# Kernel tuning notes

Hardware: AMD Instinct MI355X
Metric: run time of the kernel (lower is better)

Reference implementation:

```python
import jax, jax.numpy as jnp
import numpy as np
from jax import lax

EPS = 0.1
MAX_ITER = 100
THRESH = 0.01
N = 4  # number of prompt ensembles


def _l2norm(x, axis):
    return x / jnp.linalg.norm(x, axis=axis, keepdims=True)


def sinkhorn(K, u, v, max_iter=MAX_ITER, thresh=THRESH):
    # K: [B, M, N], u: [B, M], v: [B, N]. Matches torch loop with early exit
    # on mean(|r - r0|) < thresh, done on-device via lax.while_loop.
    dt = K.dtype
    r0 = jnp.ones_like(u)
    c0 = jnp.ones_like(v)

    def cond(state):
        _, _, i, err = state
        return jnp.logical_and(i < max_iter, err >= thresh)

    def body(state):
        r, c, i, _ = state
        r_new = u / jnp.einsum('bmn,bn->bm', K, c)
        c_new = v / jnp.einsum('bmn,bm->bn', K, r_new)
        err = jnp.mean(jnp.abs(r_new - r))
        return (r_new, c_new, i + 1, err)

    r, c, _, _ = lax.while_loop(cond, body, (r0, c0, jnp.int32(0), jnp.asarray(jnp.inf, dt)))
    # T = outer(r, c) * K
    return r[:, :, None] * c[:, None, :] * K


def setup_inputs() -> dict:
    key = jax.random.key(0)
    k1, k2, k3 = jax.random.split(key, 3)
    M, b, d = 196, 32, 512
    n_cls = 1000
    return {
        'image_features': jax.random.normal(k1, (M, b, d), dtype=jnp.float32),
        'image_feature_pool': jax.random.normal(k2, (b, d), dtype=jnp.float32),
        'text_features': jax.random.normal(k3, (N * n_cls, d), dtype=jnp.float32),
        'logit_scale': jnp.asarray(np.log(1.0 / 0.07), dtype=jnp.float32),
    }


def reference(image_features, image_feature_pool, text_features, logit_scale):
    M, b, d = image_features.shape
    n_cls = text_features.shape[0] // N

    tf = text_features.reshape(N, n_cls, d)
    text_feature_pool = tf.mean(axis=0)

    imf = _l2norm(image_features, axis=2)          # [M, b, d]
    img_pool = _l2norm(image_feature_pool, axis=1)  # [b, d]
    tfn = _l2norm(tf, axis=2)                       # [N, n_cls, d]
    txt_pool = _l2norm(text_feature_pool, axis=1)   # [n_cls, d]

    # sim: [M, N, b, n_cls] -> [M, N, b*n_cls] -> [B, M, N]
    sim = jnp.einsum('mbd,ncd->mnbc', imf, tfn)
    sim = sim.reshape(M, N, b * n_cls).transpose(2, 0, 1)
    wdist = 1.0 - sim

    B = b * n_cls
    xx = jnp.full((B, M), 1.0 / M, dtype=sim.dtype)
    yy = jnp.full((B, N), 1.0 / N, dtype=sim.dtype)

    # torch.no_grad() around Sinkhorn -> stop gradients into the iteration
    K = jnp.exp(-lax.stop_gradient(wdist) / EPS)
    T = sinkhorn(K, xx, yy)

    sim_op = jnp.sum(T * sim, axis=(1, 2)).reshape(b, n_cls)

    ls = jnp.exp(logit_scale)
    logits = ls * (img_pool @ txt_pool.T)
    logits2 = 0.5 * (ls * sim_op) + 0.5 * logits
    return logits2
```

## Files before the change

kernel.cpp:

```cpp
#include <hip/hip_runtime.h>
#include <hip/hip_bf16.h>

#define MB 6272
#define NC 4000
#define DD 512
#define NCLS 1000
#define NB 32000
#define NITER 6
#define SK_STRIDE 68

typedef __attribute__((ext_vector_type(8))) short short8;
typedef __attribute__((ext_vector_type(4))) float f32x4;
typedef __attribute__((ext_vector_type(2))) float f32x2;

__device__ __forceinline__ float bflo(unsigned u) { return __builtin_bit_cast(float, u << 16); }
__device__ __forceinline__ float bfhi(unsigned u) { return __builtin_bit_cast(float, u & 0xFFFF0000u); }
__device__ __forceinline__ float frcp(float x) { return __builtin_amdgcn_rcpf(x); }

__device__ __forceinline__ unsigned short f2bf(float x) {
  unsigned u = __builtin_bit_cast(unsigned, x);
  u += 0x7FFFu + ((u >> 16) & 1u);
  return (unsigned short)(u >> 16);
}

__device__ __forceinline__ bool is_fp32_mode(const void* lsp) {
  const unsigned short u = *(const unsigned short*)lsp;
  const float v = __builtin_bit_cast(float, (unsigned)u << 16);
  return !(v > 2.55f && v < 2.77f);
}

__device__ __forceinline__ void gl_lds16(const unsigned short* g, unsigned short* l) {
  __builtin_amdgcn_global_load_lds(
      (const __attribute__((address_space(1))) void*)g,
      (__attribute__((address_space(3))) void*)l, 16, 0, 0);
}

__global__ __launch_bounds__(256) void prep(const void* __restrict__ imgf,
                                            const void* __restrict__ imgp,
                                            const void* __restrict__ txtf,
                                            const void* __restrict__ lsp,
                                            float* __restrict__ rnAT, float* __restrict__ rnB,
                                            float* __restrict__ imgpool,
                                            float* __restrict__ txtpool,
                                            unsigned short* __restrict__ Ab,
                                            unsigned short* __restrict__ Bb) {
  const bool f32 = is_fp32_mode(lsp);
  const int w = threadIdx.x >> 6;
  const int lane = threadIdx.x & 63;
  const int row = blockIdx.x * 4 + w;
  const int d0 = lane * 8;

  float v[8];
  auto load8f = [&](const void* base, int srow) {
    if (f32) {
      const float4 a = *reinterpret_cast<const float4*>((const float*)base + (size_t)srow * DD + d0);
      const float4 b = *reinterpret_cast<const float4*>((const float*)base + (size_t)srow * DD + d0 + 4);
      v[0] = a.x; v[1] = a.y; v[2] = a.z; v[3] = a.w;
      v[4] = b.x; v[5] = b.y; v[6] = b.z; v[7] = b.w;
    } else {
      const uint4 u = *reinterpret_cast<const uint4*>((const unsigned short*)base + (size_t)srow * DD + d0);
      v[0] = bflo(u.x); v[1] = bfhi(u.x); v[2] = bflo(u.y); v[3] = bfhi(u.y);
      v[4] = bflo(u.z); v[5] = bfhi(u.z); v[6] = bflo(u.w); v[7] = bfhi(u.w);
    }
  };

  int mode;
  unsigned short* dst16 = nullptr;
  float* dstf = nullptr;
  int outidx = 0;
  if (row < MB) {
    load8f(imgf, row); mode = 0; dst16 = Ab + (size_t)row * DD + d0;
    outidx = (row & 31) * 208 + (row >> 5);
  } else if (row < MB + NC) {
    const int j = row - MB;
    load8f(txtf, (j & 3) * NCLS + (j >> 2)); mode = 1;
    dst16 = Bb + (size_t)j * DD + d0; outidx = j;
  } else if (row < MB + NC + 32) {
    const int b = row - MB - NC;
    load8f(imgp, b); mode = 2; dstf = imgpool + (size_t)b * DD + d0;
  } else {
    const int cc = row - (MB + NC + 32);
    float acc8[8] = {0, 0, 0, 0, 0, 0, 0, 0};
#pragma unroll
    for (int n = 0; n < 4; ++n) {
      load8f(txtf, n * NCLS + cc);
#pragma unroll
      for (int i = 0; i < 8; ++i) acc8[i] += v[i];
    }
#pragma unroll
    for (int i = 0; i < 8; ++i) v[i] = acc8[i] * 0.25f;
    mode = 3; dstf = txtpool + (size_t)cc * DD + d0;
  }

  float ss = 0.f;
#pragma unroll
  for (int i = 0; i < 8; ++i) ss += v[i] * v[i];
#pragma unroll
  for (int off = 1; off < 64; off <<= 1) ss += __shfl_xor(ss, off);
  const float rn = rsqrtf(ss);

  if (mode <= 1) {
    if (f32) {
      union { uint4 u; unsigned short h[8]; } r;
#pragma unroll
      for (int i = 0; i < 8; ++i) r.h[i] = f2bf(v[i]);
      *reinterpret_cast<uint4*>(dst16) = r.u;
    }
    if (lane == 0) (mode == 0 ? rnAT : rnB)[outidx] = rn;
  } else {
    float4 a, b;
    a.x = v[0] * rn; a.y = v[1] * rn; a.z = v[2] * rn; a.w = v[3] * rn;
    b.x = v[4] * rn; b.y = v[5] * rn; b.z = v[6] * rn; b.w = v[7] * rn;
    *reinterpret_cast<float4*>(dstf) = a;
    *reinterpret_cast<float4*>(dstf + 4) = b;
  }
}

__global__ __launch_bounds__(256, 3) void gemm_sink(const unsigned short* __restrict__ Ab,
                                                    const unsigned short* __restrict__ Bb,
                                                    const void* __restrict__ imgf,
                                                    const void* __restrict__ txtf,
                                                    const float* __restrict__ rnAT,
                                                    const float* __restrict__ rnB,
                                                    const float* __restrict__ imgpool,
                                                    const float* __restrict__ txtpool,
                                                    const void* __restrict__ lsp,
                                                    void* __restrict__ out) {
  __shared__ unsigned short shm[17408];
  __shared__ float rnAs[208];

  const int t = threadIdx.x;
  const int lane = t & 63;
  const int w = t >> 6;
  const int wg = blockIdx.x;
  const int b = (wg & 7) * 4 + ((wg >> 3) & 3);
  const int y = wg >> 5;
  const int quad = lane >> 4, l16 = lane & 15;

  const bool f32m = is_fp32_mode(lsp);
  const unsigned short* __restrict__ Asrc = f32m ? Ab : (const unsigned short*)imgf;
  const unsigned short* __restrict__ Bsrc = f32m ? Bb : (const unsigned short*)txtf;

  const int mbase = (w == 0) ? 0 : (3 * w + 1);
  const int nmt = (w == 0) ? 4 : 3;

  if (t < 208) rnAs[t] = rnAT[b * 208 + t];

  const unsigned short* asrc[3];
#pragma unroll
  for (int r = 0; r < 3; ++r) {
    const int g = r * 256 + t;
    const int rr = g >> 2;
    const int seg = g & 3;
    const int sg = (seg ^ (rr & 3)) * 8;
    asrc[r] = Asrc + (size_t)(rr * 32 + b) * DD + sg;
  }
  const int xrr = 192 + (lane >> 2);
  const int xseg = lane & 3;
  const int xsg = (xseg ^ (xrr & 3)) * 8;
  const int xarow = xrr < 196 ? xrr : 195;
  const unsigned short* axsrc = Asrc + (size_t)(xarow * 32 + b) * DD + xsg;
  const unsigned short* bsrc;
  {
    const int rr = t >> 2;
    const int seg = t & 3;
    const int sg = (seg ^ (rr & 3)) * 8;
    const int jg0 = y * 64 + rr;
    const int jg = jg0 < NC ? jg0 : NC - 1;
    const int brow = f32m ? jg : ((jg & 3) * NCLS + (jg >> 2));
    bsrc = Bsrc + (size_t)brow * DD + sg;
  }

  f32x4 acc[4][4];
#pragma unroll
  for (int i = 0; i < 4; ++i)
#pragma unroll
    for (int jt = 0; jt < 4; ++jt) acc[i][jt] = (f32x4)0.f;

  unsigned short* const buf0 = shm;
  unsigned short* const buf1 = shm + 8704;

  auto stage = [&](unsigned short* buf, int koff) {
#pragma unroll
    for (int r = 0; r < 3; ++r)
      gl_lds16(asrc[r] + koff, buf + (size_t)(r * 256 + w * 64) * 8);
    if (w == 0) gl_lds16(axsrc + koff, buf + (size_t)768 * 8);
    gl_lds16(bsrc + koff, buf + 6656 + (size_t)(w * 64) * 8);
  };

  auto compute = [&](const unsigned short* cb) {
    const unsigned short* Bsx = cb + 6656;
    short8 bfr[4];
#pragma unroll
    for (int jt = 0; jt < 4; ++jt) {
      const int rwb = jt * 16 + l16;
      bfr[jt] = *reinterpret_cast<const short8*>(&Bsx[rwb * 32 + (quad ^ (rwb & 3)) * 8]);
    }
    __builtin_amdgcn_s_setprio(1);
#pragma unroll
    for (int i = 0; i < 4; ++i) {
      if (i < nmt) {
        const int rw = (mbase + i) * 16 + l16;
        const short8 af = *reinterpret_cast<const short8*>(&cb[rw * 32 + (quad ^ (rw & 3)) * 8]);
#pragma unroll
        for (int jt = 0; jt < 4; ++jt)
          acc[i][jt] = __builtin_amdgcn_mfma_f32_16x16x32_bf16(af, bfr[jt], acc[i][jt], 0, 0, 0);
      }
    }
    __builtin_amdgcn_s_setprio(0);
  };

  stage(buf0, 0);
  asm volatile("s_waitcnt vmcnt(0)" ::: "memory");
  __syncthreads();

#pragma unroll 1
  for (int kt = 0; kt < 16; kt += 2) {
    stage(buf1, (kt + 1) * 32);
    compute(buf0);
    asm volatile("s_waitcnt vmcnt(0)" ::: "memory");
    __builtin_amdgcn_s_barrier();
    if (kt < 14) stage(buf0, (kt + 2) * 32);
    compute(buf1);
    asm volatile("s_waitcnt vmcnt(0)" ::: "memory");
    __builtin_amdgcn_s_barrier();
  }

  {
    float rbv[4];
#pragma unroll
    for (int jt = 0; jt < 4; ++jt) {
      const int jg = y * 64 + jt * 16 + l16;
      rbv[jt] = jg < NC ? rnB[jg] : 1.0f;
    }
#pragma unroll
    for (int i = 0; i < 4; ++i) {
      if (i < nmt) {
#pragma unroll
        for (int jt = 0; jt < 4; ++jt) {
          const int jl = jt * 16 + l16;
#pragma unroll
          for (int reg = 0; reg < 4; ++reg) {
            const int m = (mbase + i) * 16 + quad * 4 + reg;
            if (m < 196) {
              const float sim = acc[i][jt][reg] * rnAs[m] * rbv[jt];
              shm[m * SK_STRIDE + jl] = f2bf(__expf(10.f * sim - 10.f));
            }
          }
        }
      }
    }
  }
  __syncthreads();

  const int pl = lane >> 4;
  const int sub = lane & 15;
  const int mstart = sub < 4 ? sub * 13 : 52 + (sub - 4) * 12;
  const int pcol = (w * 4 + pl) * 4;

  uint2 kk[13];
#pragma unroll
  for (int i = 0; i < 13; ++i) {
    const int m = mstart + i;
    const int mc = m < 196 ? m : 195;
    kk[i] = *reinterpret_cast<const uint2*>(&shm[mc * SK_STRIDE + pcol]);
  }

  f32x2 cA = {1.f, 1.f}, cB = {1.f, 1.f};
  for (int it = 0; it < NITER - 1; ++it) {
    f32x2 SA = {0.f, 0.f}, SB = {0.f, 0.f};
#pragma unroll
    for (int i = 0; i < 13; ++i) {
      if (i < 12 || sub < 4) {
        f32x2 kA = {bflo(kk[i].x), bfhi(kk[i].x)};
        f32x2 kB = {bflo(kk[i].y), bfhi(kk[i].y)};
        const f32x2 pr = kA * cA + kB * cB;
        const float rv = (1.0f / 196.0f) * frcp(pr.x + pr.y);
        const f32x2 rvv = {rv, rv};
        SA += kA * rvv;
        SB += kB * rvv;
      }
    }
    SA.x += __shfl_xor(SA.x, 1); SA.x += __shfl_xor(SA.x, 2); SA.x += __shfl_xor(SA.x, 4); SA.x += __shfl_xor(SA.x, 8);
    SA.y += __shfl_xor(SA.y, 1); SA.y += __shfl_xor(SA.y, 2); SA.y += __shfl_xor(SA.y, 4); SA.y += __shfl_xor(SA.y, 8);
    SB.x += __shfl_xor(SB.x, 1); SB.x += __shfl_xor(SB.x, 2); SB.x += __shfl_xor(SB.x, 4); SB.x += __shfl_xor(SB.x, 8);
    SB.y += __shfl_xor(SB.y, 1); SB.y += __shfl_xor(SB.y, 2); SB.y += __shfl_xor(SB.y, 4); SB.y += __shfl_xor(SB.y, 8);
    cA.x = 0.25f * frcp(SA.x); cA.y = 0.25f * frcp(SA.y);
    cB.x = 0.25f * frcp(SB.x); cB.y = 0.25f * frcp(SB.y);
  }

  f32x2 SA = {0.f, 0.f}, SB = {0.f, 0.f}, WA = {0.f, 0.f}, WB = {0.f, 0.f};
#pragma unroll
  for (int i = 0; i < 13; ++i) {
    if (i < 12 || sub < 4) {
      f32x2 kA = {bflo(kk[i].x), bfhi(kk[i].x)};
      f32x2 kB = {bflo(kk[i].y), bfhi(kk[i].y)};
      const f32x2 pr = kA * cA + kB * cB;
      const float rv = (1.0f / 196.0f) * frcp(pr.x + pr.y);
      const f32x2 rvv = {rv, rv};
      const f32x2 tA = kA * rvv, tB = kB * rvv;
      SA += tA; SB += tB;
      const f32x2 lgA = {__logf(kA.x), __logf(kA.y)};
      const f32x2 lgB = {__logf(kB.x), __logf(kB.y)};
      const f32x2 one = {1.f, 1.f}, tenth = {0.1f, 0.1f};
      WA += tA * (one + tenth * lgA);
      WB += tB * (one + tenth * lgB);
    }
  }
  SA.x += __shfl_xor(SA.x, 1); SA.x += __shfl_xor(SA.x, 2); SA.x += __shfl_xor(SA.x, 4); SA.x += __shfl_xor(SA.x, 8);
  SA.y += __shfl_xor(SA.y, 1); SA.y += __shfl_xor(SA.y, 2); SA.y += __shfl_xor(SA.y, 4); SA.y += __shfl_xor(SA.y, 8);
  SB.x += __shfl_xor(SB.x, 1); SB.x += __shfl_xor(SB.x, 2); SB.x += __shfl_xor(SB.x, 4); SB.x += __shfl_xor(SB.x, 8);
  SB.y += __shfl_xor(SB.y, 1); SB.y += __shfl_xor(SB.y, 2); SB.y += __shfl_xor(SB.y, 4); SB.y += __shfl_xor(SB.y, 8);
  WA.x += __shfl_xor(WA.x, 1); WA.x += __shfl_xor(WA.x, 2); WA.x += __shfl_xor(WA.x, 4); WA.x += __shfl_xor(WA.x, 8);
  WA.y += __shfl_xor(WA.y, 1); WA.y += __shfl_xor(WA.y, 2); WA.y += __shfl_xor(WA.y, 4); WA.y += __shfl_xor(WA.y, 8);
  WB.x += __shfl_xor(WB.x, 1); WB.x += __shfl_xor(WB.x, 2); WB.x += __shfl_xor(WB.x, 4); WB.x += __shfl_xor(WB.x, 8);
  WB.y += __shfl_xor(WB.y, 1); WB.y += __shfl_xor(WB.y, 2); WB.y += __shfl_xor(WB.y, 4); WB.y += __shfl_xor(WB.y, 8);
  const float simop = (0.25f * frcp(SA.x)) * WA.x + (0.25f * frcp(SA.y)) * WA.y +
                      (0.25f * frcp(SB.x)) * WB.x + (0.25f * frcp(SB.y)) * WB.y;

  const int cg = y * 16 + (w * 4 + pl);
  const int cgc = cg < NCLS ? cg : NCLS - 1;
  const float4* ip4 = reinterpret_cast<const float4*>(imgpool + (size_t)b * DD);
  const float4* tp4 = reinterpret_cast<const float4*>(txtpool + (size_t)cgc * DD);
  float dot = 0.f;
#pragma unroll
  for (int i = 0; i < 8; ++i) {
    const float4 a = ip4[sub * 8 + i];
    const float4 v = tp4[sub * 8 + i];
    dot += (a.x * v.x + a.y * v.y) + (a.z * v.z + a.w * v.w);
  }
  dot += __shfl_xor(dot, 1); dot += __shfl_xor(dot, 2); dot += __shfl_xor(dot, 4); dot += __shfl_xor(dot, 8);

  if (sub == 0 && cg < NCLS) {
    const float lsv = f32m ? *(const float*)lsp : bflo(*(const unsigned short*)lsp);
    const float val = 0.5f * __expf(lsv) * (simop + dot);
    const int p = b * NCLS + cg;
    if (f32m) ((float*)out)[p] = val;
    else ((unsigned short*)out)[p] = f2bf(val);
  }
}

extern "C" void kernel_launch(void* const* d_in, const int* in_sizes, int n_in,
                              void* d_out, int out_size, void* d_ws, size_t ws_size,
                              hipStream_t stream) {
  const void* imgf = d_in[0];
  const void* imgp = d_in[1];
  const void* txtf = d_in[2];
  const void* lsp  = d_in[3];

  const size_t need = (size_t)32 * 208 * 4 + NC * 4 + 32 * DD * 4 + NCLS * DD * 4 +
                      (size_t)MB * DD * 2 + (size_t)NC * DD * 2;
  const bool ok = (n_in == 4) && in_sizes[0] == MB * DD && in_sizes[1] == 32 * DD &&
                  in_sizes[2] == NC * DD && in_sizes[3] == 1 && out_size == NB &&
                  ws_size >= need;
  if (!ok) return;

  char* w = (char*)d_ws;
  float* rnAT = (float*)w;                 w += (size_t)32 * 208 * 4;
  float* rnB = (float*)w;                  w += NC * 4;
  float* imgpool = (float*)w;              w += 32 * DD * 4;
  float* txtpool = (float*)w;              w += NCLS * DD * 4;
  unsigned short* Ab = (unsigned short*)w; w += (size_t)MB * DD * 2;
  unsigned short* Bb = (unsigned short*)w; w += (size_t)NC * DD * 2;

  prep<<<dim3(2826), dim3(256), 0, stream>>>(imgf, imgp, txtf, lsp, rnAT, rnB,
                                             imgpool, txtpool, Ab, Bb);
  gemm_sink<<<dim3(2016), dim3(256), 0, stream>>>(Ab, Bb, imgf, txtf, rnAT, rnB,
                                                  imgpool, txtpool, lsp, d_out);
}
```

Before: 142.0 us.

## Deepen GEMM K-loop to four-slot LDS ring with prefetch distance two

Replaces the double-buffered LDS pipeline, which waited for all loads with vmcnt(0) every step, with a 4-slot ring buffer. Loads are prefetched two K-steps ahead, and each step uses partial vmcnt waits so that newer loads can stay in flight. The goal is to hide global-to-LDS latency better. In exchange, LDS use doubles and launch bounds drop from 3 to 2 blocks per CU, which lowers occupancy.

```diff
diff --git a/kernel.cpp b/kernel.cpp
--- a/kernel.cpp
+++ b/kernel.cpp
@@ -8,6 +8,7 @@
 #define NB 32000
 #define NITER 6
 #define SK_STRIDE 68
+#define SLOT 8704
 
 typedef __attribute__((ext_vector_type(8))) short short8;
 typedef __attribute__((ext_vector_type(4))) float f32x4;
@@ -116,7 +117,7 @@
   }
 }
 
-__global__ __launch_bounds__(256, 3) void gemm_sink(const unsigned short* __restrict__ Ab,
+__global__ __launch_bounds__(256, 2) void gemm_sink(const unsigned short* __restrict__ Ab,
                                                     const unsigned short* __restrict__ Bb,
                                                     const void* __restrict__ imgf,
                                                     const void* __restrict__ txtf,
@@ -126,7 +127,7 @@
                                                     const float* __restrict__ txtpool,
                                                     const void* __restrict__ lsp,
                                                     void* __restrict__ out) {
-  __shared__ unsigned short shm[17408];
+  __shared__ unsigned short shm[4 * SLOT];
   __shared__ float rnAs[208];
 
   const int t = threadIdx.x;
@@ -177,9 +178,6 @@
 #pragma unroll
     for (int jt = 0; jt < 4; ++jt) acc[i][jt] = (f32x4)0.f;
 
-  unsigned short* const buf0 = shm;
-  unsigned short* const buf1 = shm + 8704;
-
   auto stage = [&](unsigned short* buf, int koff) {
 #pragma unroll
     for (int r = 0; r < 3; ++r)
@@ -210,21 +208,27 @@
     __builtin_amdgcn_s_setprio(0);
   };
 
-  stage(buf0, 0);
-  asm volatile("s_waitcnt vmcnt(0)" ::: "memory");
+  stage(shm + 0 * SLOT, 0);
+  stage(shm + 1 * SLOT, 32);
+
+#pragma unroll
+  for (int k = 0; k < 16; ++k) {
+    if (k + 2 < 16) stage(shm + (size_t)((k + 2) & 3) * SLOT, (k + 2) * 32);
+    __builtin_amdgcn_sched_barrier(0);
+    if (k < 14) {
+      if (w == 0) asm volatile("s_waitcnt vmcnt(10)" ::: "memory");
+      else        asm volatile("s_waitcnt vmcnt(8)" ::: "memory");
+    } else if (k == 14) {
+      if (w == 0) asm volatile("s_waitcnt vmcnt(5)" ::: "memory");
+      else        asm volatile("s_waitcnt vmcnt(4)" ::: "memory");
+    } else {
+      asm volatile("s_waitcnt vmcnt(0)" ::: "memory");
+    }
+    __builtin_amdgcn_sched_barrier(0);
+    __builtin_amdgcn_s_barrier();
+    compute(shm + (size_t)(k & 3) * SLOT);
+  }
   __syncthreads();
-
-#pragma unroll 1
-  for (int kt = 0; kt < 16; kt += 2) {
-    stage(buf1, (kt + 1) * 32);
-    compute(buf0);
-    asm volatile("s_waitcnt vmcnt(0)" ::: "memory");
-    __builtin_amdgcn_s_barrier();
-    if (kt < 14) stage(buf0, (kt + 2) * 32);
-    compute(buf1);
-    asm volatile("s_waitcnt vmcnt(0)" ::: "memory");
-    __builtin_amdgcn_s_barrier();
-  }
 
   {
     float rbv[4];
```

Result: slower. 160.9 us (+13.3%).
